# Performance work log

Hardware: AMD Instinct MI355X
Metric: run time of the kernel (lower is better)

## Reference

```python
import jax, jax.numpy as jnp
import numpy as np

B, N, K, DIM = 128, 512, 12, 128


def setup_inputs() -> dict:
    key = jax.random.key(0)
    ks = jax.random.split(key, 8)
    inv = 1.0 / np.sqrt(DIM)
    return {
        "self_vectors": jax.random.normal(ks[0], (B, N, DIM), dtype=jnp.float32),
        "neighbor_vector": jax.random.normal(ks[1], (B, N, K, DIM), dtype=jnp.float32),
        "neighbor_weight": jax.random.uniform(ks[2], (B, N, K), dtype=jnp.float32),
        "extra_vector": jax.random.normal(ks[3], (B, N, DIM), dtype=jnp.float32),
        "masks": jnp.ones((B, N), dtype=jnp.int32),
        "batch_size": B,
        "w_1": jax.random.uniform(ks[4], (DIM + 1, DIM), dtype=jnp.float32, minval=-inv, maxval=inv),
        "w_2": jax.random.uniform(ks[5], (DIM, 1), dtype=jnp.float32, minval=-inv, maxval=inv),
        "w_3": jax.random.uniform(ks[6], (2 * DIM, DIM), dtype=jnp.float32, minval=-inv, maxval=inv),
    }


def reference(self_vectors, neighbor_vector, neighbor_weight, extra_vector,
              masks, batch_size, w_1, w_2, w_3):
    dim = self_vectors.shape[-1]
    # [B,N,K,dim+1]: broadcast-multiply extra against neighbors, append edge weight
    feat = jnp.concatenate(
        [extra_vector[:, :, None, :] * neighbor_vector,
         neighbor_weight[..., None]], axis=-1)
    alpha = jnp.einsum('bnkf,fd->bnkd', feat, w_1)          # [B,N,K,dim]
    alpha = jax.nn.leaky_relu(alpha, negative_slope=0.2)
    alpha = jnp.einsum('bnkd,do->bnk', alpha, w_2)          # [B,N,K]
    alpha = jax.nn.softmax(alpha, axis=-1)[..., None]       # [B,N,K,1]
    agg = jnp.sum(alpha * neighbor_vector, axis=-2)         # [B,N,dim]
    out = jnp.concatenate([self_vectors, agg], axis=-1)     # [B,N,2*dim]
    # dropout p=0.0 / eval mode -> identity
    out = jnp.einsum('bnf,fd->bnd', out, w_3)
    out = out.reshape(batch_size, -1, dim)
    return jax.nn.relu(out)
```

## Files before the change

### kernel.cpp

```cpp
#include <hip/hip_runtime.h>

#define KK 12
#define DIM 128
#define BNTOT 65536

typedef __attribute__((ext_vector_type(8))) short bf16x8;
typedef __attribute__((ext_vector_type(4))) float floatx4;

static __device__ __forceinline__ unsigned short f2bf(float x) {
  unsigned u = __float_as_uint(x);
  unsigned r = (u + 0x7fffu + ((u >> 16) & 1u)) >> 16;
  return (unsigned short)r;
}
static __device__ __forceinline__ unsigned pk2(float a, float b) {
  return (unsigned)f2bf(a) | ((unsigned)f2bf(b) << 16);
}

__global__ __launch_bounds__(256) void k1_attn(
    const float* __restrict__ nbr,
    const float* __restrict__ nw,
    const float* __restrict__ extra,
    const float* __restrict__ w1,
    const float* __restrict__ w2,
    float* __restrict__ aggout)
{
  __shared__ unsigned short w1t[128][136];
  __shared__ float w1last[128];
  __shared__ float w2s[128];
  __shared__ float slds[4][16];

  const int tid = threadIdx.x;
  for (int idx = tid; idx < 128 * 128; idx += 256) {
    int k = idx >> 7, n = idx & 127;
    w1t[n][k] = f2bf(w1[idx]);
  }
  if (tid < 128) { w1last[tid] = w1[16384 + tid]; w2s[tid] = w2[tid]; }
  __syncthreads();

  const int wave = tid >> 6, lane = tid & 63;
  const int m = lane & 15;
  const int quad = lane >> 4;

  for (int it = 0; it < 4; ++it) {
    const int bn = blockIdx.x * 16 + wave * 4 + it;
    const float* nb_bn = nbr + (size_t)bn * (KK * DIM);
    const float* ex_bn = extra + (size_t)bn * DIM;

    bf16x8 afrag[4];
#pragma unroll
    for (int s = 0; s < 4; ++s) {
      const int f0 = s * 32 + quad * 8;
      float4 e0 = *(const float4*)(ex_bn + f0);
      float4 e1 = *(const float4*)(ex_bn + f0 + 4);
      float4 n0 = make_float4(0.f, 0.f, 0.f, 0.f), n1 = n0;
      if (m < KK) {
        n0 = *(const float4*)(nb_bn + m * DIM + f0);
        n1 = *(const float4*)(nb_bn + m * DIM + f0 + 4);
      }
      union { bf16x8 v; unsigned u[4]; } pk;
      pk.u[0] = pk2(e0.x * n0.x, e0.y * n0.y);
      pk.u[1] = pk2(e0.z * n0.z, e0.w * n0.w);
      pk.u[2] = pk2(e1.x * n1.x, e1.y * n1.y);
      pk.u[3] = pk2(e1.z * n1.z, e1.w * n1.w);
      afrag[s] = pk.v;
    }

    floatx4 acc[8];
#pragma unroll
    for (int nt = 0; nt < 8; ++nt) acc[nt] = (floatx4){0.f, 0.f, 0.f, 0.f};
#pragma unroll
    for (int s = 0; s < 4; ++s) {
      const int f0 = s * 32 + quad * 8;
#pragma unroll
      for (int nt = 0; nt < 8; ++nt) {
        bf16x8 bfrag = *(const bf16x8*)&w1t[nt * 16 + m][f0];
        acc[nt] = __builtin_amdgcn_mfma_f32_16x16x32_bf16(afrag[s], bfrag, acc[nt], 0, 0, 0);
      }
    }

    float wrow[4];
#pragma unroll
    for (int r = 0; r < 4; ++r) {
      int row = quad * 4 + r;
      wrow[r] = (row < KK) ? nw[bn * KK + row] : 0.f;
    }
    float part[4] = {0.f, 0.f, 0.f, 0.f};
#pragma unroll
    for (int nt = 0; nt < 8; ++nt) {
      int col = nt * 16 + m;
      float wl = w1last[col], w2c = w2s[col];
#pragma unroll
      for (int r = 0; r < 4; ++r) {
        float v = acc[nt][r] + wrow[r] * wl;
        v = (v > 0.f) ? v : 0.2f * v;
        part[r] += v * w2c;
      }
    }
#pragma unroll
    for (int r = 0; r < 4; ++r) {
      float p = part[r];
      p += __shfl_xor(p, 1); p += __shfl_xor(p, 2);
      p += __shfl_xor(p, 4); p += __shfl_xor(p, 8);
      part[r] = p;
    }
    if (m == 0) {
#pragma unroll
      for (int r = 0; r < 4; ++r) slds[wave][quad * 4 + r] = part[r];
    }
    __syncthreads();

    float sc[KK], p[KK];
    float mx = -1e30f;
#pragma unroll
    for (int k = 0; k < KK; ++k) { sc[k] = slds[wave][k]; mx = fmaxf(mx, sc[k]); }
    float psum = 0.f;
#pragma unroll
    for (int k = 0; k < KK; ++k) { p[k] = __expf(sc[k] - mx); psum += p[k]; }
    const float inv = 1.f / psum;

    const int half = lane >> 5;
    const int dq = (lane & 31) * 4;
    float4 a4 = make_float4(0.f, 0.f, 0.f, 0.f);
    if (half == 0) {
#pragma unroll
      for (int k = 0; k < 6; ++k) {
        float4 nv = *(const float4*)(nb_bn + k * DIM + dq);
        a4.x += p[k] * nv.x; a4.y += p[k] * nv.y;
        a4.z += p[k] * nv.z; a4.w += p[k] * nv.w;
      }
    } else {
#pragma unroll
      for (int k = 6; k < 12; ++k) {
        float4 nv = *(const float4*)(nb_bn + k * DIM + dq);
        a4.x += p[k] * nv.x; a4.y += p[k] * nv.y;
        a4.z += p[k] * nv.z; a4.w += p[k] * nv.w;
      }
    }
    a4.x += __shfl_xor(a4.x, 32);
    a4.y += __shfl_xor(a4.y, 32);
    a4.z += __shfl_xor(a4.z, 32);
    a4.w += __shfl_xor(a4.w, 32);
    if (half == 0) {
      float4 o = make_float4(a4.x * inv, a4.y * inv, a4.z * inv, a4.w * inv);
      *(float4*)(aggout + (size_t)bn * DIM + dq) = o;
    }
  }
}

__global__ __launch_bounds__(256) void k2_out(
    const float* __restrict__ selfv,
    const float* __restrict__ agg,
    const float* __restrict__ w3,
    float* __restrict__ out)
{
  __shared__ unsigned short w3t[128 * 256];
  const int tid = threadIdx.x;
  for (int idx = tid; idx < 256 * 128; idx += 256) {
    int k = idx >> 7, n = idx & 127;
    int pos = (((k >> 3) ^ (n & 31)) << 3) | (k & 7);
    w3t[n * 256 + pos] = f2bf(w3[idx]);
  }
  __syncthreads();

  const int wave = tid >> 6, lane = tid & 63;
  const int m = lane & 15, quad = lane >> 4;

  for (int it = 0; it < 2; ++it) {
    const int rowbase = blockIdx.x * 128 + it * 64 + wave * 16;
    const float* xs = selfv + (size_t)(rowbase + m) * DIM;
    const float* xa = agg + (size_t)(rowbase + m) * DIM;
    floatx4 acc[8];
#pragma unroll
    for (int nt = 0; nt < 8; ++nt) acc[nt] = (floatx4){0.f, 0.f, 0.f, 0.f};
#pragma unroll
    for (int s = 0; s < 8; ++s) {
      const int k0 = s * 32 + quad * 8;
      const float* src = (s < 4) ? (xs + k0) : (xa + (k0 - 128));
      float4 x0 = *(const float4*)src;
      float4 x1 = *(const float4*)(src + 4);
      union { bf16x8 v; unsigned u[4]; } pk;
      pk.u[0] = pk2(x0.x, x0.y);
      pk.u[1] = pk2(x0.z, x0.w);
      pk.u[2] = pk2(x1.x, x1.y);
      pk.u[3] = pk2(x1.z, x1.w);
#pragma unroll
      for (int nt = 0; nt < 8; ++nt) {
        int n = nt * 16 + m;
        int bk = (((s * 4 + quad) ^ (n & 31)) << 3);
        bf16x8 bfrag = *(const bf16x8*)&w3t[n * 256 + bk];
        acc[nt] = __builtin_amdgcn_mfma_f32_16x16x32_bf16(pk.v, bfrag, acc[nt], 0, 0, 0);
      }
    }
#pragma unroll
    for (int nt = 0; nt < 8; ++nt) {
      int col = nt * 16 + m;
#pragma unroll
      for (int r = 0; r < 4; ++r) {
        int orow = rowbase + quad * 4 + r;
        out[(size_t)orow * DIM + col] = fmaxf(acc[nt][r], 0.f);
      }
    }
  }
}

extern "C" void kernel_launch(void* const* d_in, const int* in_sizes, int n_in,
                              void* d_out, int out_size, void* d_ws, size_t ws_size,
                              hipStream_t stream) {
  const float* selfv = (const float*)d_in[0];
  const float* nbr   = (const float*)d_in[1];
  const float* nw    = (const float*)d_in[2];
  const float* extra = (const float*)d_in[3];
  const float* w1 = (const float*)d_in[6];
  const float* w2 = (const float*)d_in[7];
  const float* w3 = (const float*)d_in[8];
  float* out = (float*)d_out;

  const size_t need = (size_t)BNTOT * DIM * sizeof(float);
  float* agg = (ws_size >= need) ? (float*)d_ws : out;

  k1_attn<<<BNTOT / 16, 256, 0, stream>>>(nbr, nw, extra, w1, w2, agg);
  k2_out<<<BNTOT / 128, 256, 0, stream>>>(selfv, agg, w3, out);
}
```

Baseline: 751.1 us.

## Prepack W3 globally, fragment-order W1 in LDS, replace LDS softmax sync with shuffles

Adds a small pre-kernel that converts W3 to bf16 once in an MFMA fragment-ready layout, so k2 reads B fragments straight from global/L2 instead of each block converting the whole W3 into LDS. k1 stores W1 in fragment order, keeps the W1 last row and w2 in registers, replaces the LDS write plus __syncthreads for the softmax scores with wave shuffles, and issues the neighbor loads for aggregation before the MFMA loop. The aim is to cut per-block setup, LDS traffic and barriers and to hide load latency. In exchange it adds one extra launch, and k2 now depends on cached global reads for its weights.

```diff
diff --git a/kernel.cpp b/kernel.cpp
--- a/kernel.cpp
+++ b/kernel.cpp
@@ -9,11 +9,22 @@
 
 static __device__ __forceinline__ unsigned short f2bf(float x) {
   unsigned u = __float_as_uint(x);
-  unsigned r = (u + 0x7fffu + ((u >> 16) & 1u)) >> 16;
-  return (unsigned short)r;
+  return (unsigned short)((u + 0x7fffu + ((u >> 16) & 1u)) >> 16);
 }
 static __device__ __forceinline__ unsigned pk2(float a, float b) {
   return (unsigned)f2bf(a) | ((unsigned)f2bf(b) << 16);
+}
+
+__device__ unsigned short g_w3pack[256 * 128];
+
+__global__ __launch_bounds__(256) void k0_pack(const float* __restrict__ w3) {
+  int idx = blockIdx.x * 256 + threadIdx.x;
+  for (; idx < 256 * 128; idx += 32 * 256) {
+    int k = idx >> 7, n = idx & 127;
+    int s = k >> 5, quad = (k >> 3) & 3, j = k & 7;
+    int nt = n >> 4, m = n & 15;
+    g_w3pack[(((nt << 3) | s) << 9) + ((quad << 4) | m) * 8 + j] = f2bf(w3[idx]);
+  }
 }
 
 __global__ __launch_bounds__(256) void k1_attn(
@@ -24,22 +35,30 @@
     const float* __restrict__ w2,
     float* __restrict__ aggout)
 {
-  __shared__ unsigned short w1t[128][136];
-  __shared__ float w1last[128];
-  __shared__ float w2s[128];
-  __shared__ float slds[4][16];
+  __shared__ unsigned short w1f[128 * 128];
 
   const int tid = threadIdx.x;
   for (int idx = tid; idx < 128 * 128; idx += 256) {
     int k = idx >> 7, n = idx & 127;
-    w1t[n][k] = f2bf(w1[idx]);
-  }
-  if (tid < 128) { w1last[tid] = w1[16384 + tid]; w2s[tid] = w2[tid]; }
+    int s = k >> 5, quad = (k >> 3) & 3, j = k & 7;
+    int nt = n >> 4, m = n & 15;
+    w1f[(((nt << 2) | s) << 9) + ((quad << 4) | m) * 8 + j] = f2bf(w1[idx]);
+  }
   __syncthreads();
 
   const int wave = tid >> 6, lane = tid & 63;
   const int m = lane & 15;
   const int quad = lane >> 4;
+
+  float wl_r[8], w2_r[8];
+#pragma unroll
+  for (int nt = 0; nt < 8; ++nt) {
+    wl_r[nt] = w1[16384 + nt * 16 + m];
+    w2_r[nt] = w2[nt * 16 + m];
+  }
+
+  const int half = lane >> 5;
+  const int dq = (lane & 31) * 4;
 
   for (int it = 0; it < 4; ++it) {
     const int bn = blockIdx.x * 16 + wave * 4 + it;
@@ -65,15 +84,19 @@
       afrag[s] = pk.v;
     }
 
+    float4 pv[6];
+#pragma unroll
+    for (int k = 0; k < 6; ++k)
+      pv[k] = *(const float4*)(nb_bn + (half * 6 + k) * DIM + dq);
+
     floatx4 acc[8];
 #pragma unroll
     for (int nt = 0; nt < 8; ++nt) acc[nt] = (floatx4){0.f, 0.f, 0.f, 0.f};
 #pragma unroll
     for (int s = 0; s < 4; ++s) {
-      const int f0 = s * 32 + quad * 8;
 #pragma unroll
       for (int nt = 0; nt < 8; ++nt) {
-        bf16x8 bfrag = *(const bf16x8*)&w1t[nt * 16 + m][f0];
+        bf16x8 bfrag = *(const bf16x8*)&w1f[(((nt << 2) | s) << 9) + lane * 8];
         acc[nt] = __builtin_amdgcn_mfma_f32_16x16x32_bf16(afrag[s], bfrag, acc[nt], 0, 0, 0);
       }
     }
@@ -87,13 +110,11 @@
     float part[4] = {0.f, 0.f, 0.f, 0.f};
 #pragma unroll
     for (int nt = 0; nt < 8; ++nt) {
-      int col = nt * 16 + m;
-      float wl = w1last[col], w2c = w2s[col];
 #pragma unroll
       for (int r = 0; r < 4; ++r) {
-        float v = acc[nt][r] + wrow[r] * wl;
+        float v = acc[nt][r] + wrow[r] * wl_r[nt];
         v = (v > 0.f) ? v : 0.2f * v;
-        part[r] += v * w2c;
+        part[r] += v * w2_r[nt];
       }
     }
 #pragma unroll
@@ -103,38 +124,26 @@
       p += __shfl_xor(p, 4); p += __shfl_xor(p, 8);
       part[r] = p;
     }
-    if (m == 0) {
-#pragma unroll
-      for (int r = 0; r < 4; ++r) slds[wave][quad * 4 + r] = part[r];
-    }
-    __syncthreads();
-
-    float sc[KK], p[KK];
+
+    float sc[KK];
+#pragma unroll
+    for (int jr = 0; jr < KK; ++jr)
+      sc[jr] = __shfl(part[jr & 3], (jr >> 2) << 4);
+
     float mx = -1e30f;
 #pragma unroll
-    for (int k = 0; k < KK; ++k) { sc[k] = slds[wave][k]; mx = fmaxf(mx, sc[k]); }
-    float psum = 0.f;
-#pragma unroll
-    for (int k = 0; k < KK; ++k) { p[k] = __expf(sc[k] - mx); psum += p[k]; }
+    for (int k = 0; k < KK; ++k) mx = fmaxf(mx, sc[k]);
+    float p12[KK], psum = 0.f;
+#pragma unroll
+    for (int k = 0; k < KK; ++k) { p12[k] = __expf(sc[k] - mx); psum += p12[k]; }
     const float inv = 1.f / psum;
 
-    const int half = lane >> 5;
-    const int dq = (lane & 31) * 4;
     float4 a4 = make_float4(0.f, 0.f, 0.f, 0.f);
-    if (half == 0) {
-#pragma unroll
-      for (int k = 0; k < 6; ++k) {
-        float4 nv = *(const float4*)(nb_bn + k * DIM + dq);
-        a4.x += p[k] * nv.x; a4.y += p[k] * nv.y;
-        a4.z += p[k] * nv.z; a4.w += p[k] * nv.w;
-      }
-    } else {
-#pragma unroll
-      for (int k = 6; k < 12; ++k) {
-        float4 nv = *(const float4*)(nb_bn + k * DIM + dq);
-        a4.x += p[k] * nv.x; a4.y += p[k] * nv.y;
-        a4.z += p[k] * nv.z; a4.w += p[k] * nv.w;
-      }
+#pragma unroll
+    for (int k = 0; k < 6; ++k) {
+      float pk = half ? p12[k + 6] : p12[k];
+      a4.x += pk * pv[k].x; a4.y += pk * pv[k].y;
+      a4.z += pk * pv[k].z; a4.w += pk * pv[k].w;
     }
     a4.x += __shfl_xor(a4.x, 32);
     a4.y += __shfl_xor(a4.y, 32);
@@ -150,55 +159,43 @@
 __global__ __launch_bounds__(256) void k2_out(
     const float* __restrict__ selfv,
     const float* __restrict__ agg,
-    const float* __restrict__ w3,
     float* __restrict__ out)
 {
-  __shared__ unsigned short w3t[128 * 256];
-  const int tid = threadIdx.x;
-  for (int idx = tid; idx < 256 * 128; idx += 256) {
-    int k = idx >> 7, n = idx & 127;
-    int pos = (((k >> 3) ^ (n & 31)) << 3) | (k & 7);
-    w3t[n * 256 + pos] = f2bf(w3[idx]);
-  }
-  __syncthreads();
-
-  const int wave = tid >> 6, lane = tid & 63;
+  const int tid = threadIdx.x, wave = tid >> 6, lane = tid & 63;
   const int m = lane & 15, quad = lane >> 4;
-
-  for (int it = 0; it < 2; ++it) {
-    const int rowbase = blockIdx.x * 128 + it * 64 + wave * 16;
-    const float* xs = selfv + (size_t)(rowbase + m) * DIM;
-    const float* xa = agg + (size_t)(rowbase + m) * DIM;
-    floatx4 acc[8];
-#pragma unroll
-    for (int nt = 0; nt < 8; ++nt) acc[nt] = (floatx4){0.f, 0.f, 0.f, 0.f};
-#pragma unroll
-    for (int s = 0; s < 8; ++s) {
-      const int k0 = s * 32 + quad * 8;
-      const float* src = (s < 4) ? (xs + k0) : (xa + (k0 - 128));
-      float4 x0 = *(const float4*)src;
-      float4 x1 = *(const float4*)(src + 4);
-      union { bf16x8 v; unsigned u[4]; } pk;
-      pk.u[0] = pk2(x0.x, x0.y);
-      pk.u[1] = pk2(x0.z, x0.w);
-      pk.u[2] = pk2(x1.x, x1.y);
-      pk.u[3] = pk2(x1.z, x1.w);
-#pragma unroll
-      for (int nt = 0; nt < 8; ++nt) {
-        int n = nt * 16 + m;
-        int bk = (((s * 4 + quad) ^ (n & 31)) << 3);
-        bf16x8 bfrag = *(const bf16x8*)&w3t[n * 256 + bk];
-        acc[nt] = __builtin_amdgcn_mfma_f32_16x16x32_bf16(pk.v, bfrag, acc[nt], 0, 0, 0);
-      }
-    }
+  const int rowbase = blockIdx.x * 64 + wave * 16;
+  const float* xs = selfv + (size_t)(rowbase + m) * DIM;
+  const float* xa = agg + (size_t)(rowbase + m) * DIM;
+
+  floatx4 acc[8];
+#pragma unroll
+  for (int nt = 0; nt < 8; ++nt) acc[nt] = (floatx4){0.f, 0.f, 0.f, 0.f};
+
+#pragma unroll
+  for (int s = 0; s < 8; ++s) {
+    const int k0 = (s & 3) * 32 + quad * 8;
+    const float* src = (s < 4) ? (xs + k0) : (xa + k0);
+    float4 x0 = *(const float4*)src;
+    float4 x1 = *(const float4*)(src + 4);
+    union { bf16x8 v; unsigned u[4]; } pk;
+    pk.u[0] = pk2(x0.x, x0.y);
+    pk.u[1] = pk2(x0.z, x0.w);
+    pk.u[2] = pk2(x1.x, x1.y);
+    pk.u[3] = pk2(x1.z, x1.w);
 #pragma unroll
     for (int nt = 0; nt < 8; ++nt) {
-      int col = nt * 16 + m;
-#pragma unroll
-      for (int r = 0; r < 4; ++r) {
-        int orow = rowbase + quad * 4 + r;
-        out[(size_t)orow * DIM + col] = fmaxf(acc[nt][r], 0.f);
-      }
+      bf16x8 bfrag = *(const bf16x8*)&g_w3pack[(((nt << 3) | s) << 9) + lane * 8];
+      acc[nt] = __builtin_amdgcn_mfma_f32_16x16x32_bf16(pk.v, bfrag, acc[nt], 0, 0, 0);
+    }
+  }
+
+#pragma unroll
+  for (int nt = 0; nt < 8; ++nt) {
+    int col = nt * 16 + m;
+#pragma unroll
+    for (int r = 0; r < 4; ++r) {
+      int orow = rowbase + quad * 4 + r;
+      out[(size_t)orow * DIM + col] = fmaxf(acc[nt][r], 0.f);
     }
   }
 }
@@ -218,6 +215,7 @@
   const size_t need = (size_t)BNTOT * DIM * sizeof(float);
   float* agg = (ws_size >= need) ? (float*)d_ws : out;
 
+  k0_pack<<<32, 256, 0, stream>>>(w3);
   k1_attn<<<BNTOT / 16, 256, 0, stream>>>(nbr, nw, extra, w1, w2, agg);
-  k2_out<<<BNTOT / 128, 256, 0, stream>>>(selfv, agg, w3, out);
-}
+  k2_out<<<BNTOT / 64, 256, 0, stream>>>(selfv, agg, out);
+}
```

New measurement: 816.8 us. 8.7% more time.
